# Performance work log

Hardware: AMD Instinct MI355X
Metric: run time of the kernel (lower is better)

The kernel has to match this reference:

```python
import jax, jax.numpy as jnp
import numpy as np

FACTOR = 1  # init factor -> top_k = int(factor * log(L))


def setup_inputs() -> dict:
    key = jax.random.key(0)
    kq, kk, kv = jax.random.split(key, 3)
    B, L, H, E = 16, 2048, 8, 64
    shape = (B, L, H, E)
    return {
        "queries": jax.random.normal(kq, shape, dtype=jnp.float32),
        "keys": jax.random.normal(kk, shape, dtype=jnp.float32),
        "values": jax.random.normal(kv, shape, dtype=jnp.float32),
    }


def reference(queries, keys, values):
    B, L, H, E = queries.shape
    # seq lens equal -> torch's pad/truncate branch is a no-op slice
    q = jnp.transpose(queries, (0, 2, 3, 1))  # [B,H,E,L]
    k = jnp.transpose(keys, (0, 2, 3, 1))
    v = jnp.transpose(values, (0, 2, 3, 1))

    # FFT-based circular cross-correlation along time
    qf = jnp.fft.rfft(q, axis=-1)
    kf = jnp.fft.rfft(k, axis=-1)
    corr = jnp.fft.irfft(qf * jnp.conj(kf), n=L, axis=-1)  # [B,H,E,L]

    top_k = int(FACTOR * np.log(L))  # static: 7 for L=2048
    mean_value = corr.mean(axis=(1, 2))  # mean over head then variates -> [B,L]
    # global (batch-averaged) top-k delays, shared across batch (training path)
    _, topk_index = jax.lax.top_k(mean_value.mean(axis=0), top_k)  # [k]
    # per-batch weights at those delays, softmax over k
    w = jax.nn.softmax(mean_value[:, topk_index], axis=-1)  # [B,k]

    # torch.roll(v, -d, -1)[..., t] == v[..., (t + d) % L]
    idx = (jnp.arange(L)[None, :] + topk_index[:, None]) % L  # [k,L]
    gathered = v[..., idx]  # [B,H,E,k,L]
    agg = jnp.einsum('bhekl,bk->bhel', gathered, w)  # weighted delay aggregation

    return jnp.transpose(agg, (0, 3, 1, 2))  # back to [B,L,H,E]
```

## Files before the change

### kernel.cpp

```cpp
#include <hip/hip_runtime.h>
#include <hip/hip_bf16.h>
#include <math.h>


#define B_ 16
#define L_ 2048
#define H_ 8
#define E_ 64
#define C_ (H_ * E_)
#define NCH (B_ * C_)
#define K_ 7

#define Z_OFF   0ull
#define S_OFF   134217728ull
#define MV_OFF  (S_OFF + 262144ull)
#define TK_OFF  (MV_OFF + 131072ull)
#define W_OFF   (TK_OFF + 64ull)

__device__ __forceinline__ float2 cadd(float2 a, float2 b) { return make_float2(a.x + b.x, a.y + b.y); }
__device__ __forceinline__ float2 csub(float2 a, float2 b) { return make_float2(a.x - b.x, a.y - b.y); }
__device__ __forceinline__ float2 cmul(float2 a, float2 b) {
  return make_float2(fmaf(a.x, b.x, -a.y * b.y), fmaf(a.x, b.y, a.y * b.x));
}
__device__ __forceinline__ float2 cis(float ang) { float s, c; sincosf(ang, &s, &c); return make_float2(c, s); }

template<int S> __device__ __forceinline__ float2 rot90(float2 z) {
  return (S < 0) ? make_float2(z.y, -z.x) : make_float2(-z.y, z.x);
}
template<int S> __device__ __forceinline__ void dft4(float2& a, float2& b, float2& c, float2& d) {
  float2 t0 = cadd(a, c), t1 = csub(a, c), t2 = cadd(b, d), t3 = rot90<S>(csub(b, d));
  a = cadd(t0, t2); c = csub(t0, t2); b = cadd(t1, t3); d = csub(t1, t3);
}
template<int S> __device__ __forceinline__ void dft8(float2 v[8]) {
  const float RT = 0.70710678118654752f;
  const float SR = (S < 0) ? -RT : RT;
  float2 a0 = cadd(v[0], v[4]), a1 = cadd(v[1], v[5]), a2 = cadd(v[2], v[6]), a3 = cadd(v[3], v[7]);
  float2 b0 = csub(v[0], v[4]), b1 = csub(v[1], v[5]), b2 = csub(v[2], v[6]), b3 = csub(v[3], v[7]);
  b1 = cmul(b1, make_float2(RT, SR));
  b2 = rot90<S>(b2);
  b3 = cmul(b3, make_float2(-RT, SR));
  dft4<S>(a0, a1, a2, a3);
  dft4<S>(b0, b1, b2, b3);
  v[0] = a0; v[2] = a1; v[4] = a2; v[6] = a3;
  v[1] = b0; v[3] = b1; v[5] = b2; v[7] = b3;
}
__device__ __forceinline__ int sg(int e) { return e + (e >> 5); }

__global__ __launch_bounds__(256) void pack_transpose_kernel(
    const float* __restrict__ q, const float* __restrict__ k,
    float2* __restrict__ z) {
  __shared__ float2 tile[32][33];
  int bi = blockIdx.x;
  int te = bi & 1;  bi >>= 1;
  int tt = bi & 63; bi >>= 6;
  int h  = bi & 7;  bi >>= 3;
  int b  = bi;
  int e0 = te * 32, t0 = tt * 32;
  int tx = threadIdx.x, ty = threadIdx.y;
#pragma unroll
  for (int j = 0; j < 4; ++j) {
    int t = t0 + ty + j * 8;
    int e = e0 + tx;
    size_t idx = ((size_t)(b * L_ + t) * H_ + h) * E_ + e;
    tile[ty + j * 8][tx] = make_float2(q[idx], k[idx]);
  }
  __syncthreads();
#pragma unroll
  for (int j = 0; j < 4; ++j) {
    int e = e0 + ty + j * 8;
    int t = t0 + tx;
    size_t o = ((size_t)((b * H_ + h) * E_ + e)) * L_ + t;
    z[o] = tile[tx][ty + j * 8];
  }
}

__global__ __launch_bounds__(256) void fft_corr_kernel(float2* __restrict__ z) {
  __shared__ float2 buf[2112];
  int t = threadIdx.x;
  int j2 = t & 31, j3 = t & 3;
  float2 tw1[7], tw2[7], tw3[7];
#pragma unroll
  for (int k = 1; k <= 7; ++k) {
    tw1[k - 1] = cis(-6.283185307179586f * (float)(t  * k) / 2048.0f);
    tw2[k - 1] = cis(-6.283185307179586f * (float)(j2 * k) / 256.0f);
    tw3[k - 1] = cis(-6.283185307179586f * (float)(j3 * k) / 32.0f);
  }
  float2 acc[8];
#pragma unroll
  for (int k = 0; k < 8; ++k) acc[k] = make_float2(0.f, 0.f);
  int cbase = blockIdx.x * 8;
  int base2 = (t >> 5) * 256 + j2;
  int base3 = (t >> 2) * 32 + j3;

  for (int c = 0; c < 8; ++c) {
    const float2* row = z + (size_t)(cbase + c) * L_;
    float2 v[8];
#pragma unroll
    for (int m = 0; m < 8; ++m) v[m] = row[t + 256 * m];
    dft8<-1>(v);
#pragma unroll
    for (int k = 1; k < 8; ++k) v[k] = cmul(v[k], tw1[k - 1]);
    __syncthreads();
#pragma unroll
    for (int k = 0; k < 8; ++k) buf[sg(t + 256 * k)] = v[k];
    __syncthreads();
#pragma unroll
    for (int m = 0; m < 8; ++m) v[m] = buf[sg(base2 + 32 * m)];
    dft8<-1>(v);
#pragma unroll
    for (int k = 1; k < 8; ++k) v[k] = cmul(v[k], tw2[k - 1]);
    __syncthreads();
#pragma unroll
    for (int k = 0; k < 8; ++k) buf[sg(base2 + 32 * k)] = v[k];
    __syncthreads();
#pragma unroll
    for (int m = 0; m < 8; ++m) v[m] = buf[sg(base3 + 4 * m)];
    dft8<-1>(v);
#pragma unroll
    for (int k = 1; k < 8; ++k) v[k] = cmul(v[k], tw3[k - 1]);
    __syncthreads();
#pragma unroll
    for (int k = 0; k < 8; ++k) buf[sg(base3 + 4 * k)] = v[k];
    __syncthreads();
    float2 u[8];
#pragma unroll
    for (int k = 0; k < 8; ++k) u[k] = buf[sg(8 * t + k)];
    dft4<-1>(u[0], u[1], u[2], u[3]);
    dft4<-1>(u[4], u[5], u[6], u[7]);
#pragma unroll
    for (int k = 0; k < 8; ++k) buf[sg(8 * t + k)] = u[k];
    __syncthreads();
#pragma unroll
    for (int k = 0; k < 8; ++k) {
      int p = 8 * t + k;
      int f = ((p >> 8) & 7) | (((p >> 5) & 7) << 3) | (((p >> 2) & 7) << 6) | ((p & 3) << 9);
      int fp = (2048 - f) & 2047;
      int pp = ((fp & 7) << 8) | (((fp >> 3) & 7) << 5) | (((fp >> 6) & 7) << 2) | ((fp >> 9) & 3);
      float2 A = u[k];
      float2 Bc = buf[sg(pp)];
      acc[k].x += 0.5f  * (Bc.x * A.y + Bc.y * A.x);
      acc[k].y += 0.25f * (A.x * A.x + A.y * A.y - Bc.x * Bc.x - Bc.y * Bc.y);
    }
  }
  __syncthreads();
#pragma unroll
  for (int k = 0; k < 8; ++k) buf[sg(8 * t + k)] = acc[k];
  __syncthreads();
  float2* part = z + (size_t)cbase * L_;
#pragma unroll
  for (int m = 0; m < 8; ++m) part[t + 256 * m] = buf[sg(t + 256 * m)];
}

__global__ __launch_bounds__(256) void reduce_S_kernel(
    const float2* __restrict__ z, float2* __restrict__ S) {
  int gid = blockIdx.x * 256 + threadIdx.x;
  int b = gid >> 11, p = gid & 2047;
  float2 s = make_float2(0.f, 0.f);
#pragma unroll 4
  for (int i = 0; i < 64; ++i) {
    float2 vv = z[(size_t)((b * 64 + i) * 8) * L_ + p];
    s.x += vv.x; s.y += vv.y;
  }
  S[gid] = s;
}

__global__ __launch_bounds__(256) void ifft_kernel(
    const float2* __restrict__ S, float* __restrict__ mv) {
  __shared__ float2 buf[2112];
  int t = threadIdx.x, b = blockIdx.x;
  int j2 = t & 31, j3 = t & 3;
  float2 tw1[7], tw2[7], tw3[7];
#pragma unroll
  for (int k = 1; k <= 7; ++k) {
    tw1[k - 1] = cis(6.283185307179586f * (float)(t  * k) / 2048.0f);
    tw2[k - 1] = cis(6.283185307179586f * (float)(j2 * k) / 256.0f);
    tw3[k - 1] = cis(6.283185307179586f * (float)(j3 * k) / 32.0f);
  }
  int base2 = (t >> 5) * 256 + j2;
  int base3 = (t >> 2) * 32 + j3;
  const float2* row = S + b * L_;
  float2 u[8];
#pragma unroll
  for (int k = 0; k < 8; ++k) u[k] = row[8 * t + k];
  dft4<1>(u[0], u[1], u[2], u[3]);
  dft4<1>(u[4], u[5], u[6], u[7]);
#pragma unroll
  for (int k = 0; k < 8; ++k) buf[sg(8 * t + k)] = u[k];
  __syncthreads();
  float2 v[8];
#pragma unroll
  for (int k = 0; k < 8; ++k) v[k] = buf[sg(base3 + 4 * k)];
#pragma unroll
  for (int k = 1; k < 8; ++k) v[k] = cmul(v[k], tw3[k - 1]);
  dft8<1>(v);
  __syncthreads();
#pragma unroll
  for (int m = 0; m < 8; ++m) buf[sg(base3 + 4 * m)] = v[m];
  __syncthreads();
#pragma unroll
  for (int k = 0; k < 8; ++k) v[k] = buf[sg(base2 + 32 * k)];
#pragma unroll
  for (int k = 1; k < 8; ++k) v[k] = cmul(v[k], tw2[k - 1]);
  dft8<1>(v);
  __syncthreads();
#pragma unroll
  for (int m = 0; m < 8; ++m) buf[sg(base2 + 32 * m)] = v[m];
  __syncthreads();
#pragma unroll
  for (int k = 0; k < 8; ++k) v[k] = buf[sg(t + 256 * k)];
#pragma unroll
  for (int k = 1; k < 8; ++k) v[k] = cmul(v[k], tw1[k - 1]);
  dft8<1>(v);
  const float scale = 1.0f / (2048.0f * 512.0f);
#pragma unroll
  for (int m = 0; m < 8; ++m) mv[b * L_ + t + 256 * m] = v[m].x * scale;
}

__global__ __launch_bounds__(256) void topk_kernel(
    const float* __restrict__ mv, int* __restrict__ topk, float* __restrict__ wts) {
  __shared__ float av[2048];
  __shared__ float rv[256];
  __shared__ int   ri[256];
  __shared__ int   sidx[K_];
  int tid = threadIdx.x;
  for (int d = tid; d < 2048; d += 256) {
    float s = 0.f;
#pragma unroll
    for (int b = 0; b < B_; ++b) s += mv[b * L_ + d];
    av[d] = s;
  }
  __syncthreads();
  for (int k = 0; k < K_; ++k) {
    float bv = -INFINITY; int bi = 0;
    for (int d = tid; d < 2048; d += 256) {
      float vv = av[d];
      if (vv > bv) { bv = vv; bi = d; }
    }
    rv[tid] = bv; ri[tid] = bi;
    __syncthreads();
    for (int off = 128; off > 0; off >>= 1) {
      if (tid < off) {
        float v2 = rv[tid + off]; int i2 = ri[tid + off];
        if (v2 > rv[tid] || (v2 == rv[tid] && i2 < ri[tid])) { rv[tid] = v2; ri[tid] = i2; }
      }
      __syncthreads();
    }
    if (tid == 0) { sidx[k] = ri[0]; av[ri[0]] = -INFINITY; }
    __syncthreads();
  }
  if (tid < K_) topk[tid] = sidx[tid];
  if (tid < B_) {
    float x[K_], m = -INFINITY;
#pragma unroll
    for (int k = 0; k < K_; ++k) { x[k] = mv[tid * L_ + sidx[k]]; m = fmaxf(m, x[k]); }
    float s = 0.f;
#pragma unroll
    for (int k = 0; k < K_; ++k) { x[k] = expf(x[k] - m); s += x[k]; }
#pragma unroll
    for (int k = 0; k < K_; ++k) wts[tid * K_ + k] = x[k] / s;
  }
}

__global__ __launch_bounds__(256) void aggregate_kernel(
    const float4* __restrict__ v4, const int* __restrict__ topk,
    const float* __restrict__ wts, float4* __restrict__ out4) {
  __shared__ int   sidx[K_];
  __shared__ float sw[B_][K_];
  int tid = threadIdx.x;
  if (tid < K_) sidx[tid] = topk[tid];
  if (tid < B_ * K_) sw[tid / K_][tid % K_] = wts[tid];
  __syncthreads();
  int idx = blockIdx.x * 256 + tid;
  int c4  = idx & 127;
  int row = idx >> 7;
  int t   = row & (L_ - 1);
  int b   = row >> 11;
  float4 acc = make_float4(0.f, 0.f, 0.f, 0.f);
#pragma unroll
  for (int k = 0; k < K_; ++k) {
    int s = t + sidx[k];
    if (s >= L_) s -= L_;
    float w = sw[b][k];
    float4 val = v4[((size_t)(b * L_ + s) << 7) + c4];
    acc.x += w * val.x; acc.y += w * val.y;
    acc.z += w * val.z; acc.w += w * val.w;
  }
  out4[idx] = acc;
}

extern "C" void kernel_launch(void* const* d_in, const int* in_sizes, int n_in,
                              void* d_out, int out_size, void* d_ws, size_t ws_size,
                              hipStream_t stream) {
  const float* q = (const float*)d_in[0];
  const float* k = (const float*)d_in[1];
  const float* v = (const float*)d_in[2];
  float* out = (float*)d_out;

  char* ws = (char*)d_ws;
  float2* z    = (float2*)(ws + Z_OFF);
  float2* S    = (float2*)(ws + S_OFF);
  float*  mv   = (float*) (ws + MV_OFF);
  int*    topk = (int*)   (ws + TK_OFF);
  float*  wts  = (float*) (ws + W_OFF);

  pack_transpose_kernel<<<B_ * H_ * (L_ / 32) * (E_ / 32), dim3(32, 8), 0, stream>>>(q, k, z);
  fft_corr_kernel<<<NCH / 8, 256, 0, stream>>>(z);
  reduce_S_kernel<<<(B_ * L_) / 256, 256, 0, stream>>>(z, S);
  ifft_kernel<<<B_, 256, 0, stream>>>(S, mv);
  topk_kernel<<<1, 256, 0, stream>>>(mv, topk, wts);
  aggregate_kernel<<<(B_ * L_ * C_ / 4) / 256, 256, 0, stream>>>(
      (const float4*)v, topk, wts, (float4*)out);
}
```

Baseline: 176.4 us.

## Vectorize pack transpose, prefetch FFT rows, shrink CPB, split reduction across groups

```diff
diff --git a/kernel.cpp b/kernel.cpp
--- a/kernel.cpp
+++ b/kernel.cpp
@@ -10,6 +10,7 @@
 #define C_ (H_ * E_)
 #define NCH (B_ * C_)
 #define K_ 7
+#define CPB 4
 
 #define Z_OFF   0ull
 #define S_OFF   134217728ull
@@ -49,28 +50,40 @@
 __global__ __launch_bounds__(256) void pack_transpose_kernel(
     const float* __restrict__ q, const float* __restrict__ k,
     float2* __restrict__ z) {
-  __shared__ float2 tile[32][33];
+  __shared__ float2 tileT[64][66];
   int bi = blockIdx.x;
-  int te = bi & 1;  bi >>= 1;
-  int tt = bi & 63; bi >>= 6;
+  int tt = bi & 31; bi >>= 5;
   int h  = bi & 7;  bi >>= 3;
   int b  = bi;
-  int e0 = te * 32, t0 = tt * 32;
-  int tx = threadIdx.x, ty = threadIdx.y;
-#pragma unroll
-  for (int j = 0; j < 4; ++j) {
-    int t = t0 + ty + j * 8;
-    int e = e0 + tx;
-    size_t idx = ((size_t)(b * L_ + t) * H_ + h) * E_ + e;
-    tile[ty + j * 8][tx] = make_float2(q[idx], k[idx]);
-  }
-  __syncthreads();
-#pragma unroll
-  for (int j = 0; j < 4; ++j) {
-    int e = e0 + ty + j * 8;
-    int t = t0 + tx;
-    size_t o = ((size_t)((b * H_ + h) * E_ + e)) * L_ + t;
-    z[o] = tile[tx][ty + j * 8];
+  int t0 = tt * 64;
+  int tid = threadIdx.x;
+
+  int e4 = tid & 15;
+  int tr = tid >> 4;
+  int cmask = (e4 & 3) << 2;
+#pragma unroll
+  for (int p = 0; p < 4; ++p) {
+    int t = tr + 16 * p;
+    size_t idx = ((size_t)(b * L_ + t0 + t) * H_ + h) * E_ + 4 * e4;
+    float4 qv = *(const float4*)(q + idx);
+    float4 kv = *(const float4*)(k + idx);
+    int tc = t ^ cmask;
+    tileT[4 * e4 + 0][tc] = make_float2(qv.x, kv.x);
+    tileT[4 * e4 + 1][tc] = make_float2(qv.y, kv.y);
+    tileT[4 * e4 + 2][tc] = make_float2(qv.z, kv.z);
+    tileT[4 * e4 + 3][tc] = make_float2(qv.w, kv.w);
+  }
+  __syncthreads();
+
+  int e = tid >> 2;
+  int s = tid & 3;
+  int rmask = ((e >> 2) & 3) << 1;
+  const float4* src = (const float4*)&tileT[e][0];
+  size_t zrow = ((size_t)((b * H_ + h) * E_ + e)) * L_ + t0;
+  float4* zp = (float4*)(z + zrow);
+#pragma unroll
+  for (int c = 0; c < 8; ++c) {
+    zp[8 * s + c] = src[(8 * s + c) ^ rmask];
   }
 }
 
@@ -79,24 +92,41 @@
   int t = threadIdx.x;
   int j2 = t & 31, j3 = t & 3;
   float2 tw1[7], tw2[7], tw3[7];
-#pragma unroll
-  for (int k = 1; k <= 7; ++k) {
-    tw1[k - 1] = cis(-6.283185307179586f * (float)(t  * k) / 2048.0f);
-    tw2[k - 1] = cis(-6.283185307179586f * (float)(j2 * k) / 256.0f);
-    tw3[k - 1] = cis(-6.283185307179586f * (float)(j3 * k) / 32.0f);
+  {
+    float2 w1 = cis(-6.283185307179586f * (float)t  / 2048.0f);
+    float2 w2 = cis(-6.283185307179586f * (float)j2 / 256.0f);
+    float2 w3 = cis(-6.283185307179586f * (float)j3 / 32.0f);
+    tw1[0] = w1; tw2[0] = w2; tw3[0] = w3;
+#pragma unroll
+    for (int k = 1; k < 7; ++k) {
+      tw1[k] = cmul(tw1[k - 1], w1);
+      tw2[k] = cmul(tw2[k - 1], w2);
+      tw3[k] = cmul(tw3[k - 1], w3);
+    }
   }
   float2 acc[8];
 #pragma unroll
   for (int k = 0; k < 8; ++k) acc[k] = make_float2(0.f, 0.f);
-  int cbase = blockIdx.x * 8;
+  int cbase = blockIdx.x * CPB;
   int base2 = (t >> 5) * 256 + j2;
   int base3 = (t >> 2) * 32 + j3;
 
-  for (int c = 0; c < 8; ++c) {
-    const float2* row = z + (size_t)(cbase + c) * L_;
+  float2 nxt[8];
+  {
+    const float2* r0 = z + (size_t)cbase * L_;
+#pragma unroll
+    for (int m = 0; m < 8; ++m) nxt[m] = r0[t + 256 * m];
+  }
+
+  for (int c = 0; c < CPB; ++c) {
     float2 v[8];
 #pragma unroll
-    for (int m = 0; m < 8; ++m) v[m] = row[t + 256 * m];
+    for (int m = 0; m < 8; ++m) v[m] = nxt[m];
+    if (c + 1 < CPB) {
+      const float2* rn = z + (size_t)(cbase + c + 1) * L_;
+#pragma unroll
+      for (int m = 0; m < 8; ++m) nxt[m] = rn[t + 256 * m];
+    }
     dft8<-1>(v);
 #pragma unroll
     for (int k = 1; k < 8; ++k) v[k] = cmul(v[k], tw1[k - 1]);
@@ -151,37 +181,54 @@
   for (int m = 0; m < 8; ++m) part[t + 256 * m] = buf[sg(t + 256 * m)];
 }
 
-__global__ __launch_bounds__(256) void reduce_S_kernel(
-    const float2* __restrict__ z, float2* __restrict__ S) {
-  int gid = blockIdx.x * 256 + threadIdx.x;
-  int b = gid >> 11, p = gid & 2047;
+__global__ __launch_bounds__(256) void reduce_R_kernel(float2* __restrict__ z) {
+  int idx = blockIdx.x * 256 + threadIdx.x;
+  int p = idx & 2047;
+  int g = (idx >> 11) & 7;
+  int b = idx >> 14;
   float2 s = make_float2(0.f, 0.f);
 #pragma unroll 4
-  for (int i = 0; i < 64; ++i) {
-    float2 vv = z[(size_t)((b * 64 + i) * 8) * L_ + p];
+  for (int i = 0; i < 16; ++i) {
+    int part = b * 128 + g * 16 + i;
+    float2 vv = z[(size_t)(part * CPB) * L_ + p];
     s.x += vv.x; s.y += vv.y;
   }
-  S[gid] = s;
+  z[(size_t)((b * 128 + g * 16) * CPB + 1) * L_ + p] = s;
 }
 
 __global__ __launch_bounds__(256) void ifft_kernel(
-    const float2* __restrict__ S, float* __restrict__ mv) {
+    const float2* __restrict__ z, float* __restrict__ mv) {
   __shared__ float2 buf[2112];
   int t = threadIdx.x, b = blockIdx.x;
   int j2 = t & 31, j3 = t & 3;
   float2 tw1[7], tw2[7], tw3[7];
-#pragma unroll
-  for (int k = 1; k <= 7; ++k) {
-    tw1[k - 1] = cis(6.283185307179586f * (float)(t  * k) / 2048.0f);
-    tw2[k - 1] = cis(6.283185307179586f * (float)(j2 * k) / 256.0f);
-    tw3[k - 1] = cis(6.283185307179586f * (float)(j3 * k) / 32.0f);
+  {
+    float2 w1 = cis(6.283185307179586f * (float)t  / 2048.0f);
+    float2 w2 = cis(6.283185307179586f * (float)j2 / 256.0f);
+    float2 w3 = cis(6.283185307179586f * (float)j3 / 32.0f);
+    tw1[0] = w1; tw2[0] = w2; tw3[0] = w3;
+#pragma unroll
+    for (int k = 1; k < 7; ++k) {
+      tw1[k] = cmul(tw1[k - 1], w1);
+      tw2[k] = cmul(tw2[k - 1], w2);
+      tw3[k] = cmul(tw3[k - 1], w3);
+    }
   }
   int base2 = (t >> 5) * 256 + j2;
   int base3 = (t >> 2) * 32 + j3;
-  const float2* row = S + b * L_;
   float2 u[8];
 #pragma unroll
-  for (int k = 0; k < 8; ++k) u[k] = row[8 * t + k];
+  for (int k = 0; k < 8; ++k) u[k] = make_float2(0.f, 0.f);
+#pragma unroll
+  for (int g = 0; g < 8; ++g) {
+    const float4* rp = (const float4*)(z + (size_t)((b * 128 + g * 16) * CPB + 1) * L_);
+#pragma unroll
+    for (int m = 0; m < 4; ++m) {
+      float4 f = rp[4 * t + m];
+      u[2 * m].x     += f.x; u[2 * m].y     += f.y;
+      u[2 * m + 1].x += f.z; u[2 * m + 1].y += f.w;
+    }
+  }
   dft4<1>(u[0], u[1], u[2], u[3]);
   dft4<1>(u[4], u[5], u[6], u[7]);
 #pragma unroll
@@ -298,15 +345,14 @@
 
   char* ws = (char*)d_ws;
   float2* z    = (float2*)(ws + Z_OFF);
-  float2* S    = (float2*)(ws + S_OFF);
   float*  mv   = (float*) (ws + MV_OFF);
   int*    topk = (int*)   (ws + TK_OFF);
   float*  wts  = (float*) (ws + W_OFF);
 
-  pack_transpose_kernel<<<B_ * H_ * (L_ / 32) * (E_ / 32), dim3(32, 8), 0, stream>>>(q, k, z);
-  fft_corr_kernel<<<NCH / 8, 256, 0, stream>>>(z);
-  reduce_S_kernel<<<(B_ * L_) / 256, 256, 0, stream>>>(z, S);
-  ifft_kernel<<<B_, 256, 0, stream>>>(S, mv);
+  pack_transpose_kernel<<<B_ * H_ * (L_ / 64), 256, 0, stream>>>(q, k, z);
+  fft_corr_kernel<<<NCH / CPB, 256, 0, stream>>>(z);
+  reduce_R_kernel<<<(B_ * 8 * L_) / 256, 256, 0, stream>>>(z);
+  ifft_kernel<<<B_, 256, 0, stream>>>(z, mv);
   topk_kernel<<<1, 256, 0, stream>>>(mv, topk, wts);
   aggregate_kernel<<<(B_ * L_ * C_ / 4) / 256, 256, 0, stream>>>(
       (const float4*)v, topk, wts, (float4*)out);
```

Result: slower. 189.8 us (+7.6%).
